# Performance work log

Hardware: AMD Instinct MI355X
Metric: run time of the kernel (lower is better)

## Reference

```python
import jax, jax.numpy as jnp
import numpy as np
import math

D_MODEL = 1024
NUM_HEADS = 16
D_K = D_MODEL // NUM_HEADS  # 64
B, S = 4, 2048


def setup_inputs() -> dict:
    key = jax.random.key(0)
    ks = jax.random.split(key, 9)
    sc = 1.0 / math.sqrt(D_MODEL)
    return {
        "x": jax.random.normal(ks[0], (B, S, D_MODEL), jnp.float32),
        "Wq": jax.random.normal(ks[1], (D_MODEL, D_MODEL), jnp.float32) * sc,
        "bq": jax.random.normal(ks[2], (D_MODEL,), jnp.float32) * 0.01,
        "Wk": jax.random.normal(ks[3], (D_MODEL, D_MODEL), jnp.float32) * sc,
        "bk": jax.random.normal(ks[4], (D_MODEL,), jnp.float32) * 0.01,
        "Wv": jax.random.normal(ks[5], (D_MODEL, D_MODEL), jnp.float32) * sc,
        "bv": jax.random.normal(ks[6], (D_MODEL,), jnp.float32) * 0.01,
        "Wo": jax.random.normal(ks[7], (D_MODEL, D_MODEL), jnp.float32) * sc,
        "bo": jax.random.normal(ks[8], (D_MODEL,), jnp.float32) * 0.01,
    }


def reference(x, Wq, bq, Wk, bk, Wv, bv, Wo, bo):
    b, s, d = x.shape
    # Linear projections (torch Linear: x @ W.T + b)
    Q = x @ Wq.T + bq
    K = x @ Wk.T + bk
    V = x @ Wv.T + bv
    # [b, s, h*d_k] -> [b, h, s, d_k]
    split = lambda t: t.reshape(b, s, NUM_HEADS, D_K).transpose(0, 2, 1, 3)
    Q, K, V = split(Q), split(K), split(V)
    # Causal mask: query i can attend to keys j <= i
    seq = jnp.arange(s)
    causal = seq[:, None] >= seq[None, :]  # [s, s]
    # Scaled dot-product attention
    scores = jnp.einsum('bhqd,bhkd->bhqk', Q, K) / math.sqrt(D_K)
    scores = jnp.where(causal, scores, -jnp.inf)
    weights = jax.nn.softmax(scores, axis=-1)
    attn = jnp.einsum('bhqk,bhkd->bhqd', weights, V)
    # [b, h, s, d_v] -> [b, s, h*d_v]
    attn = attn.transpose(0, 2, 1, 3).reshape(b, s, NUM_HEADS * D_K)
    return attn @ Wo.T + bo
```

## Files before the change

kernel.cpp:

```cpp
#include <hip/hip_runtime.h>
#include <hip/hip_bf16.h>


typedef unsigned short u16;
typedef unsigned int u32;
typedef __attribute__((ext_vector_type(2))) unsigned int uint2v;
typedef __attribute__((ext_vector_type(4))) unsigned int uint4v;
typedef __attribute__((ext_vector_type(4))) short short4v;
typedef __attribute__((ext_vector_type(8))) short short8;
typedef __attribute__((ext_vector_type(4))) float f32x4;
typedef __attribute__((ext_vector_type(16))) float f32x16;

#define KDIM   1024
#define S_LEN  2048
#define NHEADS 16
#define DK     64
#define NEG_BIG (-30000.0f)
#define QSCALE 0.18033688011112043f

__device__ __forceinline__ u16 f2bf(float f) {
  unsigned u = __float_as_uint(f);
  return (u16)((u + 0x7FFFu + ((u >> 16) & 1u)) >> 16);
}
__device__ __forceinline__ u32 pkbf(float a, float b) {
  u32 ua = __float_as_uint(a) + 0x8000u;
  u32 ub = __float_as_uint(b) + 0x8000u;
  return __builtin_amdgcn_perm(ub, ua, 0x07060302u);
}
__device__ __forceinline__ void gl_lds16(const u16* g, u16* l) {
  __builtin_amdgcn_global_load_lds((const __attribute__((address_space(1))) void*)g,
                                   (__attribute__((address_space(3))) void*)l, 16, 0, 0);
}

__global__ __launch_bounds__(256) void cvt_kernel(
    const float* __restrict__ x,  const float* __restrict__ Wq,
    const float* __restrict__ Wk, const float* __restrict__ Wv,
    u16* __restrict__ xb, u16* __restrict__ wqb,
    u16* __restrict__ wkb, u16* __restrict__ wvb) {
  const int NX = 2097152, NW = 262144;
  const int total = NX + 3 * NW;
  for (int i = blockIdx.x * 256 + threadIdx.x; i < total; i += gridDim.x * 256) {
    const float* src; u16* dst; int off;
    if (i < NX)               { src = x;  dst = xb;  off = i; }
    else if (i < NX + NW)     { src = Wq; dst = wqb; off = i - NX; }
    else if (i < NX + 2 * NW) { src = Wk; dst = wkb; off = i - NX - NW; }
    else                      { src = Wv; dst = wvb; off = i - NX - 2 * NW; }
    f32x4 v = *(const f32x4*)(src + (size_t)off * 4);
    short4v o;
    o[0] = (short)f2bf(v[0]); o[1] = (short)f2bf(v[1]);
    o[2] = (short)f2bf(v[2]); o[3] = (short)f2bf(v[3]);
    *(short4v*)(dst + (size_t)off * 4) = o;
  }
}

__global__ __launch_bounds__(256) void cvt_wo(const float* __restrict__ W,
                                              u16* __restrict__ out) {
  const int i = blockIdx.x * 256 + threadIdx.x;
  f32x4 v = *(const f32x4*)(W + (size_t)i * 4);
  short4v o;
  o[0] = (short)f2bf(v[0]); o[1] = (short)f2bf(v[1]);
  o[2] = (short)f2bf(v[2]); o[3] = (short)f2bf(v[3]);
  *(short4v*)(out + (size_t)i * 4) = o;
}

template <int MODE>
__device__ __forceinline__ void gemm_body(const u16* __restrict__ A,
                                          const u16* __restrict__ B,
                                          const float* __restrict__ bias,
                                          void* __restrict__ outv) {
  extern __shared__ __align__(16) u16 smem[];
  u16* As0 = smem;
  u16* As1 = smem + 4096;
  u16* Bs0 = smem + 8192;
  u16* Bs1 = smem + 12288;
  const int tid = threadIdx.x;
  const int wave = tid >> 6, lane = tid & 63;
  const int quad = lane >> 4, l16 = lane & 15;
  const int wy = wave >> 1, wx = wave & 1;
  const int m0 = blockIdx.x * 128, n0 = blockIdx.y * 128;

  f32x4 acc[4][4];
#pragma unroll
  for (int i = 0; i < 4; i++)
#pragma unroll
    for (int j = 0; j < 4; j++) acc[i][j] = (f32x4){0.f, 0.f, 0.f, 0.f};

  const int srow = wave * 16 + (lane >> 2);
  const int scol = (lane & 3) * 8;
  const u16* gA0 = A + (size_t)(m0 + srow) * KDIM + scol;
  const u16* gA1 = gA0 + (size_t)64 * KDIM;
  const u16* gB0 = B + (size_t)(n0 + srow) * KDIM + scol;
  const u16* gB1 = gB0 + (size_t)64 * KDIM;
  const int soff = srow * 32 + scol;

  for (int k = 0; k < KDIM; k += 64) {
    __syncthreads();
    gl_lds16(gA0 + k,      &As0[soff]);
    gl_lds16(gA0 + k + 32, &As1[soff]);
    gl_lds16(gA1 + k,      &As0[soff + 2048]);
    gl_lds16(gA1 + k + 32, &As1[soff + 2048]);
    gl_lds16(gB0 + k,      &Bs0[soff]);
    gl_lds16(gB0 + k + 32, &Bs1[soff]);
    gl_lds16(gB1 + k,      &Bs0[soff + 2048]);
    gl_lds16(gB1 + k + 32, &Bs1[soff + 2048]);
    __syncthreads();
#pragma unroll
    for (int h = 0; h < 2; h++) {
      const u16* Ap = h ? As1 : As0;
      const u16* Bp = h ? Bs1 : Bs0;
      short8 af[4], bfr[4];
#pragma unroll
      for (int i = 0; i < 4; i++)
        af[i] = *(const short8*)&Ap[(wy * 64 + i * 16 + l16) * 32 + quad * 8];
#pragma unroll
      for (int j = 0; j < 4; j++)
        bfr[j] = *(const short8*)&Bp[(wx * 64 + j * 16 + l16) * 32 + quad * 8];
#pragma unroll
      for (int i = 0; i < 4; i++)
#pragma unroll
        for (int j = 0; j < 4; j++) {
          if (MODE == 2)
            acc[i][j] = __builtin_amdgcn_mfma_f32_16x16x32_bf16(af[i], bfr[j], acc[i][j], 0, 0, 0);
          else
            acc[i][j] = __builtin_amdgcn_mfma_f32_16x16x32_bf16(bfr[j], af[i], acc[i][j], 0, 0, 0);
        }
    }
  }

  if (MODE == 0 || MODE == 1) {
#pragma unroll
    for (int j = 0; j < 4; j++) {
      const int colb = n0 + wx * 64 + j * 16 + quad * 4;
      const int h = colb >> 6, d0 = colb & 63;
      const f32x4 bv4 = *(const f32x4*)&bias[colb];
#pragma unroll
      for (int i = 0; i < 4; i++) {
        const int row = m0 + wy * 64 + i * 16 + l16;
        const int b = row >> 11, s = row & 2047;
        float v0 = acc[i][j][0] + bv4[0], v1 = acc[i][j][1] + bv4[1];
        float v2 = acc[i][j][2] + bv4[2], v3 = acc[i][j][3] + bv4[3];
        if (MODE == 0) { v0 *= QSCALE; v1 *= QSCALE; v2 *= QSCALE; v3 *= QSCALE; }
        uint2v pk = {pkbf(v0, v1), pkbf(v2, v3)};
        if (MODE == 0) {
          *(uint2v*)&((u16*)outv)[(((size_t)(b * NHEADS + h)) * S_LEN + s) * DK + d0] = pk;
        } else {
          *(uint2v*)&((u16*)outv)[((((size_t)(b * NHEADS + h)) * 32 + (s >> 6)) * 8 +
                                   (d0 >> 3)) * 512 + (s & 63) * 8 + (d0 & 7)] = pk;
        }
      }
    }
  } else if (MODE == 2) {
#pragma unroll
    for (int j = 0; j < 4; j++) {
      const int col = n0 + wx * 64 + j * 16 + l16;
      const int h = col >> 6, d = col & 63;
      const float bvs = bias[col];
#pragma unroll
      for (int i = 0; i < 4; i++) {
        const int rowb = m0 + wy * 64 + i * 16 + quad * 4;
        const int b = rowb >> 11, s0 = rowb & 2047;
        uint2v pk = {pkbf(acc[i][j][0] + bvs, acc[i][j][1] + bvs),
                     pkbf(acc[i][j][2] + bvs, acc[i][j][3] + bvs)};
        *(uint2v*)&((u16*)outv)[((((size_t)(b * NHEADS + h)) * 32 + (s0 >> 6)) * 8 +
                                 ((s0 >> 3) & 7)) * 512 + (size_t)d * 8 + (s0 & 7)] = pk;
      }
    }
  } else {
#pragma unroll
    for (int j = 0; j < 4; j++) {
      const int colb = n0 + wx * 64 + j * 16 + quad * 4;
      const f32x4 bv4 = *(const f32x4*)&bias[colb];
#pragma unroll
      for (int i = 0; i < 4; i++) {
        const int row = m0 + wy * 64 + i * 16 + l16;
        f32x4 v = {acc[i][j][0] + bv4[0], acc[i][j][1] + bv4[1],
                   acc[i][j][2] + bv4[2], acc[i][j][3] + bv4[3]};
        *(f32x4*)&((float*)outv)[(size_t)row * 1024 + colb] = v;
      }
    }
  }
}

__global__ __launch_bounds__(256) void qkv_gemm(
    const u16* __restrict__ xb,
    const u16* __restrict__ wqb, const float* __restrict__ bq,
    const u16* __restrict__ wkb, const float* __restrict__ bk,
    const u16* __restrict__ wvb, const float* __restrict__ bv,
    u16* __restrict__ qb, u16* __restrict__ kb, u16* __restrict__ vb) {
  if (blockIdx.z == 0)      gemm_body<0>(xb, wqb, bq, qb);
  else if (blockIdx.z == 1) gemm_body<1>(xb, wkb, bk, kb);
  else                      gemm_body<2>(xb, wvb, bv, vb);
}

__global__ __launch_bounds__(256) void out_gemm(const u16* __restrict__ A,
                                                const u16* __restrict__ wob,
                                                const float* __restrict__ bo,
                                                float* __restrict__ out) {
  gemm_body<3>(A, wob, bo, out);
}

__global__ __launch_bounds__(256) void attn_kernel(const u16* __restrict__ Qb,
                                                   const u16* __restrict__ Kb,
                                                   const u16* __restrict__ Vb,
                                                   u16* __restrict__ Ob) {
  __shared__ __align__(16) u16 Ks[2][8][512];
  __shared__ __align__(16) u16 Vs[2][8][512];
  const int bh = blockIdx.x;
  const int qt = (int)gridDim.y - 1 - (int)blockIdx.y;
  const int tid = threadIdx.x, wave = tid >> 6, lane = tid & 63;
  const int l32 = lane & 31, hi = lane >> 5;
  const u16* Qh = Qb + (size_t)bh * S_LEN * DK;
  const u16* Kg = Kb + (size_t)bh * S_LEN * DK;
  const u16* Vg = Vb + (size_t)bh * S_LEN * DK;
  const int qw = qt * 128 + wave * 32;
  const int qrow = qw + l32;

  short8 qf[4];
#pragma unroll
  for (int c = 0; c < 4; c++)
    qf[c] = *(const short8*)&Qh[(size_t)qrow * DK + c * 16 + hi * 8];

  short8 ones;
#pragma unroll
  for (int i = 0; i < 8; i++) ones[i] = (short)0x3F80;

  f32x16 zz;
#pragma unroll
  for (int i = 0; i < 16; i++) zz[i] = 0.f;
  f32x16 o0 = zz, o1 = zz, l_acc = zz;

  const int sg = wave * 2;
  const u16* srcK = Kg + sg * 512 + lane * 8;
  const u16* srcV = Vg + sg * 512 + lane * 8;
  u16* dstK0 = &Ks[0][sg][lane * 8];
  u16* dstK1 = &Ks[1][sg][lane * 8];
  u16* dstV0 = &Vs[0][sg][lane * 8];
  u16* dstV1 = &Vs[1][sg][lane * 8];

  for (int t = 0; t <= qt; ++t) {
    const size_t g0 = (size_t)(2 * t) * 4096, g1 = (size_t)(2 * t + 1) * 4096;
    __syncthreads();
    gl_lds16(srcK + g0, dstK0);        gl_lds16(srcK + g0 + 512, dstK0 + 512);
    gl_lds16(srcK + g1, dstK1);        gl_lds16(srcK + g1 + 512, dstK1 + 512);
    gl_lds16(srcV + g0, dstV0);        gl_lds16(srcV + g0 + 512, dstV0 + 512);
    gl_lds16(srcV + g1, dstV1);        gl_lds16(srcV + g1 + 512, dstV1 + 512);
    __syncthreads();

#pragma unroll
    for (int kb = 0; kb < 4; ++kb) {
      const int kbase = t * 128 + kb * 32;
      if (kbase > qw) break;

      f32x16 st = zz;
#pragma unroll
      for (int c = 0; c < 4; c++) {
        const short8 kf = *(const short8*)
            &Ks[kb >> 1][c * 2 + hi][((kb & 1) * 32 + l32) * 8];
        st = __builtin_amdgcn_mfma_f32_32x32x16_bf16(kf, qf[c], st, 0, 0, 0);
      }

      if (kbase == qw) {
#pragma unroll
        for (int r = 0; r < 16; r++) {
          const int ko = (r & 3) + 8 * (r >> 2) + 4 * hi;
          st[r] = (ko > l32) ? NEG_BIG : st[r];
        }
      }

      float e[16];
#pragma unroll
      for (int r = 0; r < 16; r++) e[r] = __builtin_amdgcn_exp2f(st[r]);

      uint2v sA0 = __builtin_amdgcn_permlane32_swap(pkbf(e[0], e[1]),  pkbf(e[4], e[5]),  false, false);
      uint2v sB0 = __builtin_amdgcn_permlane32_swap(pkbf(e[2], e[3]),  pkbf(e[6], e[7]),  false, false);
      uint2v sA1 = __builtin_amdgcn_permlane32_swap(pkbf(e[8], e[9]),  pkbf(e[12], e[13]), false, false);
      uint2v sB1 = __builtin_amdgcn_permlane32_swap(pkbf(e[10], e[11]), pkbf(e[14], e[15]), false, false);
      union { uint4v u; short8 s; } p0, p1;
      p0.u = (uint4v){sA0[0], sB0[0], sA0[1], sB0[1]};
      p1.u = (uint4v){sA1[0], sB1[0], sA1[1], sB1[1]};
      const short8 pa0 = p0.s, pa1 = p1.s;

      l_acc = __builtin_amdgcn_mfma_f32_32x32x16_bf16(pa0, ones, l_acc, 0, 0, 0);
      l_acc = __builtin_amdgcn_mfma_f32_32x32x16_bf16(pa1, ones, l_acc, 0, 0, 0);

#pragma unroll
      for (int cc = 0; cc < 2; cc++) {
        const int kc = kb * 2 + cc;
        const short8 pa = cc ? pa1 : pa0;
        const short8 vf0 = *(const short8*)&Vs[kc >> 2][(kc & 3) * 2 + hi][l32 * 8];
        const short8 vf1 = *(const short8*)&Vs[kc >> 2][(kc & 3) * 2 + hi][(32 + l32) * 8];
        o0 = __builtin_amdgcn_mfma_f32_32x32x16_bf16(pa, vf0, o0, 0, 0, 0);
        o1 = __builtin_amdgcn_mfma_f32_32x32x16_bf16(pa, vf1, o1, 0, 0, 0);
      }
    }
  }

  const int b = bh >> 4, h = bh & 15;
#pragma unroll
  for (int r = 0; r < 16; r++) {
    const int s = qw + (r & 3) + 8 * (r >> 2) + 4 * hi;
    const float inv = __builtin_amdgcn_rcpf(l_acc[r]);
    const unsigned v0 = __float_as_uint(o0[r] * inv) + 0x8000u;
    const unsigned v1 = __float_as_uint(o1[r] * inv) + 0x8000u;
    u16* p = &Ob[((size_t)b * S_LEN + s) * 1024 + h * DK + l32];
    p[0]  = (u16)(v0 >> 16);
    p[32] = (u16)(v1 >> 16);
  }
}

extern "C" void kernel_launch(void* const* d_in, const int* in_sizes, int n_in,
                              void* d_out, int out_size, void* d_ws, size_t ws_size,
                              hipStream_t stream) {
  const float* x  = (const float*)d_in[0];
  const float* Wq = (const float*)d_in[1];
  const float* bq = (const float*)d_in[2];
  const float* Wk = (const float*)d_in[3];
  const float* bk = (const float*)d_in[4];
  const float* Wv = (const float*)d_in[5];
  const float* bv = (const float*)d_in[6];
  const float* Wo = (const float*)d_in[7];
  const float* bo = (const float*)d_in[8];

  u16* outh = (u16*)d_out;
  u16* wsh  = (u16*)d_ws;
  u16* qb  = outh;
  u16* xb  = outh + (size_t)8388608;
  u16* kb  = wsh;
  u16* vb  = wsh + (size_t)8388608;
  u16* ab  = wsh + (size_t)16777216;
  u16* wqb = ab;
  u16* wkb = wqb + (size_t)1048576;
  u16* wvb = wkb + (size_t)1048576;
  u16* wob = kb;

  cvt_kernel<<<dim3(2048), 256, 0, stream>>>(x, Wq, Wk, Wv, xb, wqb, wkb, wvb);
  qkv_gemm<<<dim3(64, 8, 3), 256, 32768, stream>>>(xb, wqb, bq, wkb, bk, wvb, bv, qb, kb, vb);
  attn_kernel<<<dim3(64, 16), 256, 0, stream>>>(qb, kb, vb, ab);
  cvt_wo<<<dim3(1024), 256, 0, stream>>>(Wo, wob);
  out_gemm<<<dim3(64, 8), 256, 32768, stream>>>(ab, wob, bo, (float*)d_out);
}
```

Before: 238.4 us.

## Use 256x128 double-buffered GEMM tiles with swizzled LDS and prefetch

Measured after the change: 257.8 us. +8.1%, slower.

```diff
diff --git a/kernel.cpp b/kernel.cpp
--- a/kernel.cpp
+++ b/kernel.cpp
@@ -64,20 +64,20 @@
 }
 
 template <int MODE>
-__device__ __forceinline__ void gemm_body(const u16* __restrict__ A,
-                                          const u16* __restrict__ B,
-                                          const float* __restrict__ bias,
-                                          void* __restrict__ outv) {
+__device__ __forceinline__ void gemm256_body(const u16* __restrict__ A,
+                                             const u16* __restrict__ B,
+                                             const float* __restrict__ bias,
+                                             void* __restrict__ outv) {
   extern __shared__ __align__(16) u16 smem[];
-  u16* As0 = smem;
-  u16* As1 = smem + 4096;
-  u16* Bs0 = smem + 8192;
-  u16* Bs1 = smem + 12288;
+  u16* const As0 = smem;
+  u16* const As1 = smem + 8192;
+  u16* const Bs0 = smem + 16384;
+  u16* const Bs1 = smem + 20480;
   const int tid = threadIdx.x;
   const int wave = tid >> 6, lane = tid & 63;
   const int quad = lane >> 4, l16 = lane & 15;
   const int wy = wave >> 1, wx = wave & 1;
-  const int m0 = blockIdx.x * 128, n0 = blockIdx.y * 128;
+  const int m0 = blockIdx.x * 256, n0 = blockIdx.y * 128;
 
   f32x4 acc[4][4];
 #pragma unroll
@@ -85,45 +85,76 @@
 #pragma unroll
     for (int j = 0; j < 4; j++) acc[i][j] = (f32x4){0.f, 0.f, 0.f, 0.f};
 
-  const int srow = wave * 16 + (lane >> 2);
-  const int scol = (lane & 3) * 8;
-  const u16* gA0 = A + (size_t)(m0 + srow) * KDIM + scol;
-  const u16* gA1 = gA0 + (size_t)64 * KDIM;
-  const u16* gB0 = B + (size_t)(n0 + srow) * KDIM + scol;
-  const u16* gB1 = gB0 + (size_t)64 * KDIM;
-  const int soff = srow * 32 + scol;
-
-  for (int k = 0; k < KDIM; k += 64) {
-    __syncthreads();
-    gl_lds16(gA0 + k,      &As0[soff]);
-    gl_lds16(gA0 + k + 32, &As1[soff]);
-    gl_lds16(gA1 + k,      &As0[soff + 2048]);
-    gl_lds16(gA1 + k + 32, &As1[soff + 2048]);
-    gl_lds16(gB0 + k,      &Bs0[soff]);
-    gl_lds16(gB0 + k + 32, &Bs1[soff]);
-    gl_lds16(gB1 + k,      &Bs0[soff + 2048]);
-    gl_lds16(gB1 + k + 32, &Bs1[soff + 2048]);
-    __syncthreads();
-#pragma unroll
-    for (int h = 0; h < 2; h++) {
-      const u16* Ap = h ? As1 : As0;
-      const u16* Bp = h ? Bs1 : Bs0;
-      short8 af[4], bfr[4];
-#pragma unroll
-      for (int i = 0; i < 4; i++)
-        af[i] = *(const short8*)&Ap[(wy * 64 + i * 16 + l16) * 32 + quad * 8];
-#pragma unroll
-      for (int j = 0; j < 4; j++)
-        bfr[j] = *(const short8*)&Bp[(wx * 64 + j * 16 + l16) * 32 + quad * 8];
-#pragma unroll
-      for (int i = 0; i < 4; i++)
-#pragma unroll
-        for (int j = 0; j < 4; j++) {
-          if (MODE == 2)
-            acc[i][j] = __builtin_amdgcn_mfma_f32_16x16x32_bf16(af[i], bfr[j], acc[i][j], 0, 0, 0);
-          else
-            acc[i][j] = __builtin_amdgcn_mfma_f32_16x16x32_bf16(bfr[j], af[i], acc[i][j], 0, 0, 0);
-        }
+  const int sr = lane >> 2, sc = lane & 3;
+  const int scs = (sc ^ ((sr >> 1) & 3)) * 8;
+  const u16* gA0 = A + (size_t)(m0 + wave * 32 + sr) * KDIM + scs;
+  const u16* gA1 = A + (size_t)(m0 + wave * 32 + 16 + sr) * KDIM + scs;
+  const u16* gB  = B + (size_t)(n0 + wave * 16 + sr) * KDIM + scs;
+  const int dA0 = (wave * 32) * 32 + lane * 8;
+  const int dA1 = dA0 + 512;
+  const int dB  = (wave * 16) * 32 + lane * 8;
+  const int fs = (quad ^ ((l16 >> 1) & 3)) * 8;
+
+  gl_lds16(gA0, As0 + dA0);
+  gl_lds16(gA1, As0 + dA1);
+  gl_lds16(gB,  Bs0 + dB);
+  asm volatile("s_waitcnt vmcnt(0)" ::: "memory");
+  __builtin_amdgcn_s_barrier();
+  asm volatile("" ::: "memory");
+
+  int cur = 0;
+  for (int t = 0; t < 32; ++t) {
+    const u16* Ab = cur ? As1 : As0;
+    const u16* Bb = cur ? Bs1 : Bs0;
+    u16* An = cur ? As0 : As1;
+    u16* Bn = cur ? Bs0 : Bs1;
+    const bool more = (t + 1 < 32);
+    const int kn = (t + 1) * 32;
+
+    short8 af[4], bf0, bf1;
+#pragma unroll
+    for (int i = 0; i < 4; i++)
+      af[i] = *(const short8*)&Ab[(wy * 64 + i * 16 + l16) * 32 + fs];
+    bf0 = *(const short8*)&Bb[(wx * 64 + l16) * 32 + fs];
+    bf1 = *(const short8*)&Bb[(wx * 64 + 16 + l16) * 32 + fs];
+    if (more) {
+      gl_lds16(gA0 + kn, An + dA0);
+      gl_lds16(gA1 + kn, An + dA1);
+    }
+    __builtin_amdgcn_s_setprio(1);
+#pragma unroll
+    for (int i = 0; i < 4; i++) {
+      if (MODE == 2) {
+        acc[i][0] = __builtin_amdgcn_mfma_f32_16x16x32_bf16(af[i], bf0, acc[i][0], 0, 0, 0);
+        acc[i][1] = __builtin_amdgcn_mfma_f32_16x16x32_bf16(af[i], bf1, acc[i][1], 0, 0, 0);
+      } else {
+        acc[i][0] = __builtin_amdgcn_mfma_f32_16x16x32_bf16(bf0, af[i], acc[i][0], 0, 0, 0);
+        acc[i][1] = __builtin_amdgcn_mfma_f32_16x16x32_bf16(bf1, af[i], acc[i][1], 0, 0, 0);
+      }
+    }
+    __builtin_amdgcn_s_setprio(0);
+
+    bf0 = *(const short8*)&Bb[(wx * 64 + 32 + l16) * 32 + fs];
+    bf1 = *(const short8*)&Bb[(wx * 64 + 48 + l16) * 32 + fs];
+    if (more) gl_lds16(gB + kn, Bn + dB);
+    __builtin_amdgcn_s_setprio(1);
+#pragma unroll
+    for (int i = 0; i < 4; i++) {
+      if (MODE == 2) {
+        acc[i][2] = __builtin_amdgcn_mfma_f32_16x16x32_bf16(af[i], bf0, acc[i][2], 0, 0, 0);
+        acc[i][3] = __builtin_amdgcn_mfma_f32_16x16x32_bf16(af[i], bf1, acc[i][3], 0, 0, 0);
+      } else {
+        acc[i][2] = __builtin_amdgcn_mfma_f32_16x16x32_bf16(bf0, af[i], acc[i][2], 0, 0, 0);
+        acc[i][3] = __builtin_amdgcn_mfma_f32_16x16x32_bf16(bf1, af[i], acc[i][3], 0, 0, 0);
+      }
+    }
+    __builtin_amdgcn_s_setprio(0);
+
+    if (more) {
+      asm volatile("s_waitcnt vmcnt(0)" ::: "memory");
+      __builtin_amdgcn_s_barrier();
+      asm volatile("" ::: "memory");
+      cur ^= 1;
     }
   }
 
@@ -181,22 +212,22 @@
   }
 }
 
-__global__ __launch_bounds__(256) void qkv_gemm(
+__global__ __launch_bounds__(512) void qkv_gemm(
     const u16* __restrict__ xb,
     const u16* __restrict__ wqb, const float* __restrict__ bq,
     const u16* __restrict__ wkb, const float* __restrict__ bk,
     const u16* __restrict__ wvb, const float* __restrict__ bv,
     u16* __restrict__ qb, u16* __restrict__ kb, u16* __restrict__ vb) {
-  if (blockIdx.z == 0)      gemm_body<0>(xb, wqb, bq, qb);
-  else if (blockIdx.z == 1) gemm_body<1>(xb, wkb, bk, kb);
-  else                      gemm_body<2>(xb, wvb, bv, vb);
-}
-
-__global__ __launch_bounds__(256) void out_gemm(const u16* __restrict__ A,
+  if (blockIdx.z == 0)      gemm256_body<0>(xb, wqb, bq, qb);
+  else if (blockIdx.z == 1) gemm256_body<1>(xb, wkb, bk, kb);
+  else                      gemm256_body<2>(xb, wvb, bv, vb);
+}
+
+__global__ __launch_bounds__(512) void out_gemm(const u16* __restrict__ A,
                                                 const u16* __restrict__ wob,
                                                 const float* __restrict__ bo,
                                                 float* __restrict__ out) {
-  gemm_body<3>(A, wob, bo, out);
+  gemm256_body<3>(A, wob, bo, out);
 }
 
 __global__ __launch_bounds__(256) void attn_kernel(const u16* __restrict__ Qb,
@@ -334,8 +365,8 @@
   u16* wob = kb;
 
   cvt_kernel<<<dim3(2048), 256, 0, stream>>>(x, Wq, Wk, Wv, xb, wqb, wkb, wvb);
-  qkv_gemm<<<dim3(64, 8, 3), 256, 32768, stream>>>(xb, wqb, bq, wkb, bk, wvb, bv, qb, kb, vb);
+  qkv_gemm<<<dim3(32, 8, 3), 512, 49152, stream>>>(xb, wqb, bq, wkb, bk, wvb, bv, qb, kb, vb);
   attn_kernel<<<dim3(64, 16), 256, 0, stream>>>(qb, kb, vb, ab);
   cvt_wo<<<dim3(1024), 256, 0, stream>>>(Wo, wob);
-  out_gemm<<<dim3(64, 8), 256, 32768, stream>>>(ab, wob, bo, (float*)d_out);
-}
+  out_gemm<<<dim3(32, 8), 512, 49152, stream>>>(ab, wob, bo, (float*)d_out);
+}
```
